# Kernel optimization log

Measured on AMD Instinct MI355X. Metric: run time of the kernel, lower is better.

The kernel has to match this reference:

```python
import jax, jax.numpy as jnp
import numpy as np

N_NODES = 50000
N_EDGES = 200000
N_GRAPHS = 1024
D = 24          # node feature dim (fixed by Set2Set(24))
E_FEAT = 8
E_HID = 128


def setup_inputs() -> dict:
    key = jax.random.key(0)
    ks = jax.random.split(key, 20)
    s = 0.1  # weight scale for numerical sanity
    inp = {
        "x": jax.random.normal(ks[0], (N_NODES, D), jnp.float32),
        "edge_attr": jax.random.normal(ks[1], (N_EDGES, E_FEAT), jnp.float32),
        # edge-network MLP: E_FEAT -> E_HID -> D*D
        "w_e1": jax.random.normal(ks[2], (E_FEAT, E_HID), jnp.float32) * s,
        "b_e1": jnp.zeros((E_HID,), jnp.float32),
        "w_e2": jax.random.normal(ks[3], (E_HID, D * D), jnp.float32) * s,
        "b_e2": jnp.zeros((D * D,), jnp.float32),
        # NNConv root weight + bias
        "root": jax.random.normal(ks[4], (D, D), jnp.float32) * s,
        "bias_conv": jnp.zeros((D,), jnp.float32),
        # Set2Set LSTM (input 2D=48, hidden D=24), torch gate order i,f,g,o
        "w_ih": jax.random.normal(ks[5], (4 * D, 2 * D), jnp.float32) * s,
        "w_hh": jax.random.normal(ks[6], (4 * D, D), jnp.float32) * s,
        "b_ih": jnp.zeros((4 * D,), jnp.float32),
        "b_hh": jnp.zeros((4 * D,), jnp.float32),
        # heads
        "w_fc2": jax.random.normal(ks[7], (2 * D, 8), jnp.float32) * s,
        "b_fc2": jnp.zeros((8,), jnp.float32),
        "w_fc3": jax.random.normal(ks[8], (8, 2), jnp.float32) * s,
        "b_fc3": jnp.zeros((2,), jnp.float32),
        "edge_index": jax.random.randint(ks[9], (2, N_EDGES), 0, N_NODES, jnp.int64),
        "batch": jnp.sort(jax.random.randint(ks[10], (N_NODES,), 0, N_GRAPHS, jnp.int64)),
    }
    return inp


def _nnconv(x, edge_attr, edge_index, w_e1, b_e1, w_e2, b_e2, root, bias_conv):
    src, dst = edge_index[0], edge_index[1]
    h = jax.nn.relu(edge_attr @ w_e1 + b_e1)
    w = (h @ w_e2 + b_e2).reshape(-1, D, D)          # [E, D_in, D_out]
    msg = jnp.einsum('ei,eio->eo', x[src], w)         # gather + per-edge matvec
    s = jax.ops.segment_sum(msg, dst, num_segments=N_NODES)
    cnt = jax.ops.segment_sum(jnp.ones((msg.shape[0],), msg.dtype), dst, num_segments=N_NODES)
    agg = s / jnp.maximum(cnt, 1.0)[:, None]          # scatter-mean
    return agg + x @ root + bias_conv


def _set2set(x, batch, w_ih, w_hh, b_ih, b_hh):
    B = N_GRAPHS
    q_star = jnp.zeros((B, 2 * D), x.dtype)
    h = jnp.zeros((B, D), x.dtype)
    c = jnp.zeros((B, D), x.dtype)
    for _ in range(3):  # processing_steps=3 (fixed small loop)
        gates = q_star @ w_ih.T + b_ih + h @ w_hh.T + b_hh
        i, f, g, o = jnp.split(gates, 4, axis=-1)
        c = jax.nn.sigmoid(f) * c + jax.nn.sigmoid(i) * jnp.tanh(g)
        h = jax.nn.sigmoid(o) * jnp.tanh(c)
        q = h                                         # [B, D]
        e = jnp.sum(x * q[batch], axis=-1)            # [N]
        e_max = jax.ops.segment_max(e, batch, num_segments=B)
        e_max = jnp.where(jnp.isfinite(e_max), e_max, 0.0)
        ex = jnp.exp(e - e_max[batch])
        denom = jax.ops.segment_sum(ex, batch, num_segments=B)
        a = ex / jnp.maximum(denom, 1e-16)[batch]     # per-graph softmax
        r = jax.ops.segment_sum(a[:, None] * x, batch, num_segments=B)
        q_star = jnp.concatenate([q, r], axis=-1)
    return q_star


def reference(x, edge_attr, w_e1, b_e1, w_e2, b_e2, root, bias_conv,
              w_ih, w_hh, b_ih, b_hh, w_fc2, b_fc2, w_fc3, b_fc3,
              edge_index, batch):
    x = _nnconv(x, edge_attr, edge_index, w_e1, b_e1, w_e2, b_e2, root, bias_conv)
    x = jax.nn.relu(x)
    x = _nnconv(x, edge_attr, edge_index, w_e1, b_e1, w_e2, b_e2, root, bias_conv)
    q_star = _set2set(x, batch, w_ih, w_hh, b_ih, b_hh)
    out = jax.nn.relu(q_star @ w_fc2 + b_fc2)
    return out @ w_fc3 + b_fc3                        # [B, 2]
```

## Files before the change

### kernel.cpp

```cpp
#include <hip/hip_runtime.h>
#include <math.h>

#define N_NODES 50000
#define N_EDGES 200000
#define N_GRAPHS 1024
#define DIM 24
#define EF 8
#define EH 128
#define DD 576
#define HSTR 136

typedef __attribute__((ext_vector_type(8))) _Float16 f16x8;
typedef __attribute__((ext_vector_type(4))) _Float16 f16x4;
typedef __attribute__((ext_vector_type(2))) _Float16 f16x2;
typedef __attribute__((ext_vector_type(4))) float float4e;
typedef _Float16 f16;

static __device__ __forceinline__ float sigm(float x) { return 1.0f / (1.0f + expf(-x)); }

__global__ void deg_kernel(const int* __restrict__ dst, int* __restrict__ deg) {
    int i = blockIdx.x * blockDim.x + threadIdx.x;
    if (i < N_EDGES) atomicAdd(&deg[dst[i]], 1);
}

__global__ __launch_bounds__(256) void bz_kernel(const float* __restrict__ w2,
                                                 const float* __restrict__ b2,
                                                 f16* __restrict__ Bz) {
    int idx = blockIdx.x * 256 + threadIdx.x;
    if (idx >= 97 * 2 * 64 * 8) return;
    int kk = idx & 7, lane = (idx >> 3) & 63, nt = (idx >> 9) & 1, p = idx >> 10;
    int q = lane >> 4, l16 = lane & 15, n = nt * 16 + l16;
    float v = 0.0f;
    if (p < 96) {
        int si = p / 24, i = p % 24;
        int k = si * 32 + q * 8 + kk;
        if (n < 24) v = w2[(size_t)k * DD + i * 24 + n];
    } else {
        int i2 = q * 8 + kk;
        if (i2 < 24 && n < 24) v = b2[i2 * 24 + n];
    }
    Bz[idx] = (f16)v;
}

__global__ __launch_bounds__(256, 4) void conv_kernel(
    const float* __restrict__ x, const float* __restrict__ ea,
    const float* __restrict__ w1, const float* __restrict__ b1,
    const f16* __restrict__ Bz,
    const int* __restrict__ src, const int* __restrict__ dst,
    float* __restrict__ agg)
{
    __shared__ f16 hs[128 * HSTR];

    const int t  = threadIdx.x;
    const int e0 = blockIdx.x * 128;

    const int lane = t & 63;
    const int wave = t >> 6;
    const int l16  = lane & 15;
    const int quad = lane >> 4;
    const int ebase = e0 + wave * 32;

    f16x2 xa[12], xb[12];
    {
        int ega = ebase + l16;      if (ega >= N_EDGES) ega = N_EDGES - 1;
        int egb = ebase + 16 + l16; if (egb >= N_EDGES) egb = N_EDGES - 1;
        const float* xra = x + (size_t)src[ega] * DIM;
        const float* xrb = x + (size_t)src[egb] * DIM;
        #pragma unroll
        for (int j4 = 0; j4 < 6; ++j4) {
            float4 va = *(const float4*)(xra + j4 * 4);
            float4 vb = *(const float4*)(xrb + j4 * 4);
            xa[j4 * 2]     = (f16x2){(f16)va.x, (f16)va.y};
            xa[j4 * 2 + 1] = (f16x2){(f16)va.z, (f16)va.w};
            xb[j4 * 2]     = (f16x2){(f16)vb.x, (f16)vb.y};
            xb[j4 * 2 + 1] = (f16x2){(f16)vb.z, (f16)vb.w};
        }
    }

    {
        const int s5 = t & 31;
        const int eb = (t >> 5) * 16;
        float wv[EF][4];
        #pragma unroll
        for (int j = 0; j < EF; ++j) {
            float4 v = *(const float4*)(w1 + j * EH + s5 * 4);
            wv[j][0] = v.x; wv[j][1] = v.y; wv[j][2] = v.z; wv[j][3] = v.w;
        }
        float4 bv = *(const float4*)(b1 + s5 * 4);
        const float bvv[4] = {bv.x, bv.y, bv.z, bv.w};
        #pragma unroll
        for (int e = 0; e < 16; ++e) {
            int eg = e0 + eb + e; if (eg >= N_EDGES) eg = N_EDGES - 1;
            const float* ear = ea + (size_t)eg * EF;
            float4 a0 = *(const float4*)ear;
            float4 a1 = *(const float4*)(ear + 4);
            const float av[EF] = {a0.x, a0.y, a0.z, a0.w, a1.x, a1.y, a1.z, a1.w};
            float r[4] = {bvv[0], bvv[1], bvv[2], bvv[3]};
            #pragma unroll
            for (int j = 0; j < EF; ++j)
                #pragma unroll
                for (int c = 0; c < 4; ++c)
                    r[c] = fmaf(av[j], wv[j][c], r[c]);
            f16x4 hq = { (f16)fmaxf(r[0], 0.0f), (f16)fmaxf(r[1], 0.0f),
                         (f16)fmaxf(r[2], 0.0f), (f16)fmaxf(r[3], 0.0f) };
            *(f16x4*)&hs[(eb + e) * HSTR + s5 * 4] = hq;
        }
    }

    const f16x8* bz = (const f16x8*)Bz + lane;
    f16x8 pb0[2], pb1[2];
    pb0[0] = bz[0];   pb1[0] = bz[64];
    pb0[1] = bz[128]; pb1[1] = bz[192];

    __syncthreads();

    float4e a00 = {0.f,0.f,0.f,0.f}, a01 = {0.f,0.f,0.f,0.f};
    float4e a10 = {0.f,0.f,0.f,0.f}, a11 = {0.f,0.f,0.f,0.f};

    #pragma unroll
    for (int si = 0; si < 4; ++si) {
        union { f16x8 v; f16x2 p[4]; } h0u, h1u;
        h0u.v = *(const f16x8*)&hs[(wave * 32 + l16) * HSTR + si * 32 + quad * 8];
        h1u.v = *(const f16x8*)&hs[(wave * 32 + 16 + l16) * HSTR + si * 32 + quad * 8];
        #pragma unroll
        for (int i = 0; i < 24; ++i) {
            const int p = si * 24 + i;
            f16x8 b0 = pb0[p & 1], b1v = pb1[p & 1];
            if (p + 2 <= 96) {
                pb0[p & 1] = bz[(p + 2) * 128];
                pb1[p & 1] = bz[(p + 2) * 128 + 64];
            }
            f16 xea = (i & 1) ? xa[i >> 1][1] : xa[i >> 1][0];
            f16 xeb = (i & 1) ? xb[i >> 1][1] : xb[i >> 1][0];
            f16x2 xa2 = {xea, xea}, xb2 = {xeb, xeb};
            union { f16x8 v; f16x2 p[4]; } a0u, a1u;
            #pragma unroll
            for (int j = 0; j < 4; ++j) {
                a0u.p[j] = h0u.p[j] * xa2;
                a1u.p[j] = h1u.p[j] * xb2;
            }
            a00 = __builtin_amdgcn_mfma_f32_16x16x32_f16(a0u.v, b0,  a00, 0, 0, 0);
            a10 = __builtin_amdgcn_mfma_f32_16x16x32_f16(a1u.v, b0,  a10, 0, 0, 0);
            a01 = __builtin_amdgcn_mfma_f32_16x16x32_f16(a0u.v, b1v, a01, 0, 0, 0);
            a11 = __builtin_amdgcn_mfma_f32_16x16x32_f16(a1u.v, b1v, a11, 0, 0, 0);
            if ((p % 12) == 11) __syncthreads();
        }
    }

    {
        union { f16x8 v; f16x2 p[4]; } a0u, a1u;
        f16x2 z2 = {(f16)0.f, (f16)0.f};
        if (quad == 0)      { a0u.p[0]=xa[0]; a0u.p[1]=xa[1]; a0u.p[2]=xa[2];  a0u.p[3]=xa[3];
                              a1u.p[0]=xb[0]; a1u.p[1]=xb[1]; a1u.p[2]=xb[2];  a1u.p[3]=xb[3];  }
        else if (quad == 1) { a0u.p[0]=xa[4]; a0u.p[1]=xa[5]; a0u.p[2]=xa[6];  a0u.p[3]=xa[7];
                              a1u.p[0]=xb[4]; a1u.p[1]=xb[5]; a1u.p[2]=xb[6];  a1u.p[3]=xb[7];  }
        else if (quad == 2) { a0u.p[0]=xa[8]; a0u.p[1]=xa[9]; a0u.p[2]=xa[10]; a0u.p[3]=xa[11];
                              a1u.p[0]=xb[8]; a1u.p[1]=xb[9]; a1u.p[2]=xb[10]; a1u.p[3]=xb[11]; }
        else                { a0u.p[0]=z2; a0u.p[1]=z2; a0u.p[2]=z2; a0u.p[3]=z2;
                              a1u.p[0]=z2; a1u.p[1]=z2; a1u.p[2]=z2; a1u.p[3]=z2; }
        a00 = __builtin_amdgcn_mfma_f32_16x16x32_f16(a0u.v, pb0[0], a00, 0, 0, 0);
        a10 = __builtin_amdgcn_mfma_f32_16x16x32_f16(a1u.v, pb0[0], a10, 0, 0, 0);
        a01 = __builtin_amdgcn_mfma_f32_16x16x32_f16(a0u.v, pb1[0], a01, 0, 0, 0);
        a11 = __builtin_amdgcn_mfma_f32_16x16x32_f16(a1u.v, pb1[0], a11, 0, 0, 0);
    }

    #pragma unroll
    for (int r = 0; r < 4; ++r) {
        int er = ebase + quad * 4 + r;
        if (er < N_EDGES) {
            int d = dst[er];
            atomicAdd(&agg[(size_t)d * DIM + l16], a00[r]);
            if (l16 < 8) atomicAdd(&agg[(size_t)d * DIM + 16 + l16], a01[r]);
        }
        int er2 = ebase + 16 + quad * 4 + r;
        if (er2 < N_EDGES) {
            int d = dst[er2];
            atomicAdd(&agg[(size_t)d * DIM + l16], a10[r]);
            if (l16 < 8) atomicAdd(&agg[(size_t)d * DIM + 16 + l16], a11[r]);
        }
    }
}

__global__ void combine_kernel(
    const float* __restrict__ x_in, const float* __restrict__ agg,
    const int* __restrict__ deg, const float* __restrict__ root,
    const float* __restrict__ bias, float* __restrict__ x_out, int do_relu)
{
    int t = blockIdx.x * blockDim.x + threadIdx.x;
    if (t >= N_NODES * DIM) return;
    int v = t / DIM, o = t % DIM;
    int dg = deg[v];
    float d = dg > 0 ? (float)dg : 1.0f;
    float a = agg[t] / d + bias[o];
    const float* xr = x_in + (size_t)v * DIM;
    #pragma unroll
    for (int i = 0; i < DIM; ++i) a = fmaf(xr[i], root[i * DIM + o], a);
    x_out[t] = do_relu ? fmaxf(a, 0.0f) : a;
}

__global__ __launch_bounds__(64) void s2s_kernel(
    const float* __restrict__ x, const int* __restrict__ batch,
    const float* __restrict__ w_ih, const float* __restrict__ w_hh,
    const float* __restrict__ b_ih, const float* __restrict__ b_hh,
    const float* __restrict__ w_fc2, const float* __restrict__ b_fc2,
    const float* __restrict__ w_fc3, const float* __restrict__ b_fc3,
    float* __restrict__ out)
{
    const int g = blockIdx.x;
    const int t = threadIdx.x;
    __shared__ float qs[48];
    __shared__ float hh[24], cc[24], gates[96], zl[8];
    __shared__ int s_lo, s_hi;

    if (t == 0) {
        int lo = 0, hi = N_NODES;
        while (lo < hi) { int m = (lo + hi) >> 1; if (batch[m] < g) lo = m + 1; else hi = m; }
        s_lo = lo;
        int lo2 = lo; hi = N_NODES;
        while (lo2 < hi) { int m = (lo2 + hi) >> 1; if (batch[m] <= g) lo2 = m + 1; else hi = m; }
        s_hi = lo2;
    }
    if (t < 48) qs[t] = 0.0f;
    if (t < 24) { hh[t] = 0.0f; cc[t] = 0.0f; }
    __syncthreads();
    const int lo = s_lo, hi = s_hi;

    for (int it = 0; it < 3; ++it) {
        for (int rr = t; rr < 96; rr += 64) {
            float a = b_ih[rr] + b_hh[rr];
            const float* wi = w_ih + (size_t)rr * 48;
            const float* wh = w_hh + (size_t)rr * 24;
            #pragma unroll
            for (int j = 0; j < 48; ++j) a = fmaf(qs[j], wi[j], a);
            #pragma unroll
            for (int j = 0; j < 24; ++j) a = fmaf(hh[j], wh[j], a);
            gates[rr] = a;
        }
        __syncthreads();
        if (t < 24) {
            float c = sigm(gates[24 + t]) * cc[t] + sigm(gates[t]) * tanhf(gates[48 + t]);
            cc[t] = c;
            float h = sigm(gates[72 + t]) * tanhf(c);
            hh[t] = h;
            qs[t] = h;
        }
        __syncthreads();

        float m_l = -INFINITY, s_l = 0.0f;
        float r_l[24];
        #pragma unroll
        for (int d = 0; d < 24; ++d) r_l[d] = 0.0f;
        for (int n = lo + t; n < hi; n += 64) {
            float xv[24];
            #pragma unroll
            for (int j = 0; j < 6; ++j)
                *(float4*)&xv[j * 4] = ((const float4*)(x + (size_t)n * DIM))[j];
            float e = 0.0f;
            #pragma unroll
            for (int d = 0; d < 24; ++d) e = fmaf(xv[d], qs[d], e);
            if (e > m_l) {
                float sc = expf(m_l - e);
                #pragma unroll
                for (int d = 0; d < 24; ++d) r_l[d] *= sc;
                s_l *= sc;
                m_l = e;
            }
            float w = expf(e - m_l);
            s_l += w;
            #pragma unroll
            for (int d = 0; d < 24; ++d) r_l[d] = fmaf(w, xv[d], r_l[d]);
        }
        float m = m_l;
        #pragma unroll
        for (int off = 32; off; off >>= 1) m = fmaxf(m, __shfl_xor(m, off));
        float fac = (m_l == -INFINITY) ? 0.0f : expf(m_l - m);
        float s = s_l * fac;
        #pragma unroll
        for (int off = 32; off; off >>= 1) s += __shfl_xor(s, off);
        float denom = fmaxf(s, 1e-16f);
        #pragma unroll
        for (int d = 0; d < 24; ++d) {
            float rv = r_l[d] * fac;
            #pragma unroll
            for (int off = 32; off; off >>= 1) rv += __shfl_xor(rv, off);
            if (t == d) qs[24 + d] = rv / denom;
        }
        __syncthreads();
    }

    if (t < 8) {
        float a = b_fc2[t];
        #pragma unroll
        for (int j = 0; j < 48; ++j) a = fmaf(qs[j], w_fc2[j * 8 + t], a);
        zl[t] = fmaxf(a, 0.0f);
    }
    __syncthreads();
    if (t < 2) {
        float a = b_fc3[t];
        #pragma unroll
        for (int k = 0; k < 8; ++k) a = fmaf(zl[k], w_fc3[k * 2 + t], a);
        out[(size_t)g * 2 + t] = a;
    }
}

extern "C" void kernel_launch(void* const* d_in, const int* in_sizes, int n_in,
                              void* d_out, int out_size, void* d_ws, size_t ws_size,
                              hipStream_t stream) {
    const float* x      = (const float*)d_in[0];
    const float* ea     = (const float*)d_in[1];
    const float* w_e1   = (const float*)d_in[2];
    const float* b_e1   = (const float*)d_in[3];
    const float* w_e2   = (const float*)d_in[4];
    const float* b_e2   = (const float*)d_in[5];
    const float* root   = (const float*)d_in[6];
    const float* bias_c = (const float*)d_in[7];
    const float* w_ih   = (const float*)d_in[8];
    const float* w_hh   = (const float*)d_in[9];
    const float* b_ih   = (const float*)d_in[10];
    const float* b_hh   = (const float*)d_in[11];
    const float* w_fc2  = (const float*)d_in[12];
    const float* b_fc2  = (const float*)d_in[13];
    const float* w_fc3  = (const float*)d_in[14];
    const float* b_fc3  = (const float*)d_in[15];
    const int*   eidx   = (const int*)d_in[16];
    const int*   batch  = (const int*)d_in[17];
    const int* esrc = eidx;
    const int* edst = eidx + N_EDGES;
    float* out = (float*)d_out;

    char* ws = (char*)d_ws;
    float* agg   = (float*)(ws);
    int*   deg   = (int*)  (ws + 4800000);
    float* x1    = (float*)(ws + 5789824);
    float* x2    = (float*)(ws + 10589824);
    f16*   Bz    = (f16*)  (ws + 15389824);

    hipMemsetAsync(ws, 0, 5000000, stream);

    deg_kernel<<<(N_EDGES + 255) / 256, 256, 0, stream>>>(edst, deg);
    bz_kernel<<<(97 * 2 * 64 * 8 + 255) / 256, 256, 0, stream>>>(w_e2, b_e2, Bz);

    conv_kernel<<<(N_EDGES + 127) / 128, 256, 0, stream>>>(x, ea, w_e1, b_e1, Bz, esrc, edst, agg);
    combine_kernel<<<(N_NODES * DIM + 255) / 256, 256, 0, stream>>>(x, agg, deg, root, bias_c, x1, 1);

    hipMemsetAsync(agg, 0, 4800000, stream);
    conv_kernel<<<(N_EDGES + 127) / 128, 256, 0, stream>>>(x1, ea, w_e1, b_e1, Bz, esrc, edst, agg);
    combine_kernel<<<(N_NODES * DIM + 255) / 256, 256, 0, stream>>>(x1, agg, deg, root, bias_c, x2, 0);

    s2s_kernel<<<N_GRAPHS, 64, 0, stream>>>(x2, batch, w_ih, w_hh, b_ih, b_hh,
                                            w_fc2, b_fc2, w_fc3, b_fc3, out);
}
```

Baseline: 301.2 us.

## Compute edge hidden layer in registers, fuse prep kernels and agg zeroing

The conv kernel no longer stages the edge-MLP hidden activations in shared memory. Each lane now recomputes its own 8 hidden values per k-slice directly from edge_attr and w_e1, which removes the LDS buffer and all __syncthreads barriers but adds redundant FMAs. The degree and Bz preparation kernels are merged into one launch, and the memset between convs is folded into combine_kernel zeroing agg as it reads it. The s2s gate matvec now uses float4 weight loads.

```diff
diff --git a/kernel.cpp b/kernel.cpp
--- a/kernel.cpp
+++ b/kernel.cpp
@@ -8,25 +8,26 @@
 #define EF 8
 #define EH 128
 #define DD 576
-#define HSTR 136
 
 typedef __attribute__((ext_vector_type(8))) _Float16 f16x8;
-typedef __attribute__((ext_vector_type(4))) _Float16 f16x4;
 typedef __attribute__((ext_vector_type(2))) _Float16 f16x2;
 typedef __attribute__((ext_vector_type(4))) float float4e;
 typedef _Float16 f16;
 
 static __device__ __forceinline__ float sigm(float x) { return 1.0f / (1.0f + expf(-x)); }
 
-__global__ void deg_kernel(const int* __restrict__ dst, int* __restrict__ deg) {
-    int i = blockIdx.x * blockDim.x + threadIdx.x;
-    if (i < N_EDGES) atomicAdd(&deg[dst[i]], 1);
-}
-
-__global__ __launch_bounds__(256) void bz_kernel(const float* __restrict__ w2,
-                                                 const float* __restrict__ b2,
-                                                 f16* __restrict__ Bz) {
-    int idx = blockIdx.x * 256 + threadIdx.x;
+__global__ __launch_bounds__(256) void prep_kernel(
+    const int* __restrict__ dst, int* __restrict__ deg,
+    const float* __restrict__ w2, const float* __restrict__ b2,
+    f16* __restrict__ Bz)
+{
+    const int b = blockIdx.x, t = threadIdx.x;
+    if (b < 782) {
+        int i = b * 256 + t;
+        if (i < N_EDGES) atomicAdd(&deg[dst[i]], 1);
+        return;
+    }
+    int idx = (b - 782) * 256 + t;
     if (idx >= 97 * 2 * 64 * 8) return;
     int kk = idx & 7, lane = (idx >> 3) & 63, nt = (idx >> 9) & 1, p = idx >> 10;
     int q = lane >> 4, l16 = lane & 15, n = nt * 16 + l16;
@@ -49,8 +50,6 @@
     const int* __restrict__ src, const int* __restrict__ dst,
     float* __restrict__ agg)
 {
-    __shared__ f16 hs[128 * HSTR];
-
     const int t  = threadIdx.x;
     const int e0 = blockIdx.x * 128;
 
@@ -60,10 +59,28 @@
     const int quad = lane >> 4;
     const int ebase = e0 + wave * 32;
 
+    const f16x8* bz = (const f16x8*)Bz + lane;
+    f16x8 pb0[2], pb1[2];
+    pb0[0] = bz[0];   pb1[0] = bz[64];
+    pb0[1] = bz[128]; pb1[1] = bz[192];
+
+    int ega = ebase + l16;      if (ega >= N_EDGES) ega = N_EDGES - 1;
+    int egb = ebase + 16 + l16; if (egb >= N_EDGES) egb = N_EDGES - 1;
+
+    float eaa[EF], eab[EF];
+    {
+        const float* pa = ea + (size_t)ega * EF;
+        const float* pb = ea + (size_t)egb * EF;
+        float4 a0 = *(const float4*)pa, a1 = *(const float4*)(pa + 4);
+        float4 b0 = *(const float4*)pb, b1_ = *(const float4*)(pb + 4);
+        eaa[0]=a0.x; eaa[1]=a0.y; eaa[2]=a0.z; eaa[3]=a0.w;
+        eaa[4]=a1.x; eaa[5]=a1.y; eaa[6]=a1.z; eaa[7]=a1.w;
+        eab[0]=b0.x; eab[1]=b0.y; eab[2]=b0.z; eab[3]=b0.w;
+        eab[4]=b1_.x; eab[5]=b1_.y; eab[6]=b1_.z; eab[7]=b1_.w;
+    }
+
     f16x2 xa[12], xb[12];
     {
-        int ega = ebase + l16;      if (ega >= N_EDGES) ega = N_EDGES - 1;
-        int egb = ebase + 16 + l16; if (egb >= N_EDGES) egb = N_EDGES - 1;
         const float* xra = x + (size_t)src[ega] * DIM;
         const float* xrb = x + (size_t)src[egb] * DIM;
         #pragma unroll
@@ -77,51 +94,39 @@
         }
     }
 
-    {
-        const int s5 = t & 31;
-        const int eb = (t >> 5) * 16;
-        float wv[EF][4];
-        #pragma unroll
-        for (int j = 0; j < EF; ++j) {
-            float4 v = *(const float4*)(w1 + j * EH + s5 * 4);
-            wv[j][0] = v.x; wv[j][1] = v.y; wv[j][2] = v.z; wv[j][3] = v.w;
-        }
-        float4 bv = *(const float4*)(b1 + s5 * 4);
-        const float bvv[4] = {bv.x, bv.y, bv.z, bv.w};
-        #pragma unroll
-        for (int e = 0; e < 16; ++e) {
-            int eg = e0 + eb + e; if (eg >= N_EDGES) eg = N_EDGES - 1;
-            const float* ear = ea + (size_t)eg * EF;
-            float4 a0 = *(const float4*)ear;
-            float4 a1 = *(const float4*)(ear + 4);
-            const float av[EF] = {a0.x, a0.y, a0.z, a0.w, a1.x, a1.y, a1.z, a1.w};
-            float r[4] = {bvv[0], bvv[1], bvv[2], bvv[3]};
-            #pragma unroll
-            for (int j = 0; j < EF; ++j)
-                #pragma unroll
-                for (int c = 0; c < 4; ++c)
-                    r[c] = fmaf(av[j], wv[j][c], r[c]);
-            f16x4 hq = { (f16)fmaxf(r[0], 0.0f), (f16)fmaxf(r[1], 0.0f),
-                         (f16)fmaxf(r[2], 0.0f), (f16)fmaxf(r[3], 0.0f) };
-            *(f16x4*)&hs[(eb + e) * HSTR + s5 * 4] = hq;
-        }
-    }
-
-    const f16x8* bz = (const f16x8*)Bz + lane;
-    f16x8 pb0[2], pb1[2];
-    pb0[0] = bz[0];   pb1[0] = bz[64];
-    pb0[1] = bz[128]; pb1[1] = bz[192];
-
-    __syncthreads();
-
     float4e a00 = {0.f,0.f,0.f,0.f}, a01 = {0.f,0.f,0.f,0.f};
     float4e a10 = {0.f,0.f,0.f,0.f}, a11 = {0.f,0.f,0.f,0.f};
 
     #pragma unroll
     for (int si = 0; si < 4; ++si) {
+        const int k0 = si * 32 + quad * 8;
+        float ha[8], hb[8];
+        {
+            float4 bv0 = *(const float4*)(b1 + k0);
+            float4 bv1 = *(const float4*)(b1 + k0 + 4);
+            ha[0]=bv0.x; ha[1]=bv0.y; ha[2]=bv0.z; ha[3]=bv0.w;
+            ha[4]=bv1.x; ha[5]=bv1.y; ha[6]=bv1.z; ha[7]=bv1.w;
+            #pragma unroll
+            for (int kk = 0; kk < 8; ++kk) hb[kk] = ha[kk];
+            #pragma unroll
+            for (int j = 0; j < EF; ++j) {
+                float4 w0 = *(const float4*)(w1 + j * EH + k0);
+                float4 w4 = *(const float4*)(w1 + j * EH + k0 + 4);
+                const float wj[8] = {w0.x, w0.y, w0.z, w0.w, w4.x, w4.y, w4.z, w4.w};
+                #pragma unroll
+                for (int kk = 0; kk < 8; ++kk) {
+                    ha[kk] = fmaf(eaa[j], wj[kk], ha[kk]);
+                    hb[kk] = fmaf(eab[j], wj[kk], hb[kk]);
+                }
+            }
+        }
         union { f16x8 v; f16x2 p[4]; } h0u, h1u;
-        h0u.v = *(const f16x8*)&hs[(wave * 32 + l16) * HSTR + si * 32 + quad * 8];
-        h1u.v = *(const f16x8*)&hs[(wave * 32 + 16 + l16) * HSTR + si * 32 + quad * 8];
+        #pragma unroll
+        for (int kk = 0; kk < 8; ++kk) {
+            ((f16*)&h0u.v)[kk] = (f16)fmaxf(ha[kk], 0.0f);
+            ((f16*)&h1u.v)[kk] = (f16)fmaxf(hb[kk], 0.0f);
+        }
+
         #pragma unroll
         for (int i = 0; i < 24; ++i) {
             const int p = si * 24 + i;
@@ -143,21 +148,18 @@
             a10 = __builtin_amdgcn_mfma_f32_16x16x32_f16(a1u.v, b0,  a10, 0, 0, 0);
             a01 = __builtin_amdgcn_mfma_f32_16x16x32_f16(a0u.v, b1v, a01, 0, 0, 0);
             a11 = __builtin_amdgcn_mfma_f32_16x16x32_f16(a1u.v, b1v, a11, 0, 0, 0);
-            if ((p % 12) == 11) __syncthreads();
         }
     }
 
     {
         union { f16x8 v; f16x2 p[4]; } a0u, a1u;
         f16x2 z2 = {(f16)0.f, (f16)0.f};
-        if (quad == 0)      { a0u.p[0]=xa[0]; a0u.p[1]=xa[1]; a0u.p[2]=xa[2];  a0u.p[3]=xa[3];
-                              a1u.p[0]=xb[0]; a1u.p[1]=xb[1]; a1u.p[2]=xb[2];  a1u.p[3]=xb[3];  }
-        else if (quad == 1) { a0u.p[0]=xa[4]; a0u.p[1]=xa[5]; a0u.p[2]=xa[6];  a0u.p[3]=xa[7];
-                              a1u.p[0]=xb[4]; a1u.p[1]=xb[5]; a1u.p[2]=xb[6];  a1u.p[3]=xb[7];  }
-        else if (quad == 2) { a0u.p[0]=xa[8]; a0u.p[1]=xa[9]; a0u.p[2]=xa[10]; a0u.p[3]=xa[11];
-                              a1u.p[0]=xb[8]; a1u.p[1]=xb[9]; a1u.p[2]=xb[10]; a1u.p[3]=xb[11]; }
-        else                { a0u.p[0]=z2; a0u.p[1]=z2; a0u.p[2]=z2; a0u.p[3]=z2;
-                              a1u.p[0]=z2; a1u.p[1]=z2; a1u.p[2]=z2; a1u.p[3]=z2; }
+        #pragma unroll
+        for (int j = 0; j < 4; ++j) {
+            int i2 = quad * 4 + j;
+            a0u.p[j] = (i2 < 12) ? xa[i2] : z2;
+            a1u.p[j] = (i2 < 12) ? xb[i2] : z2;
+        }
         a00 = __builtin_amdgcn_mfma_f32_16x16x32_f16(a0u.v, pb0[0], a00, 0, 0, 0);
         a10 = __builtin_amdgcn_mfma_f32_16x16x32_f16(a1u.v, pb0[0], a10, 0, 0, 0);
         a01 = __builtin_amdgcn_mfma_f32_16x16x32_f16(a0u.v, pb1[0], a01, 0, 0, 0);
@@ -182,9 +184,10 @@
 }
 
 __global__ void combine_kernel(
-    const float* __restrict__ x_in, const float* __restrict__ agg,
+    const float* __restrict__ x_in, float* __restrict__ agg,
     const int* __restrict__ deg, const float* __restrict__ root,
-    const float* __restrict__ bias, float* __restrict__ x_out, int do_relu)
+    const float* __restrict__ bias, float* __restrict__ x_out,
+    int do_relu, int zero_agg)
 {
     int t = blockIdx.x * blockDim.x + threadIdx.x;
     if (t >= N_NODES * DIM) return;
@@ -192,6 +195,7 @@
     int dg = deg[v];
     float d = dg > 0 ? (float)dg : 1.0f;
     float a = agg[t] / d + bias[o];
+    if (zero_agg) agg[t] = 0.0f;
     const float* xr = x_in + (size_t)v * DIM;
     #pragma unroll
     for (int i = 0; i < DIM; ++i) a = fmaf(xr[i], root[i * DIM + o], a);
@@ -231,9 +235,17 @@
             const float* wi = w_ih + (size_t)rr * 48;
             const float* wh = w_hh + (size_t)rr * 24;
             #pragma unroll
-            for (int j = 0; j < 48; ++j) a = fmaf(qs[j], wi[j], a);
-            #pragma unroll
-            for (int j = 0; j < 24; ++j) a = fmaf(hh[j], wh[j], a);
+            for (int j4 = 0; j4 < 12; ++j4) {
+                float4 w = *(const float4*)(wi + j4 * 4);
+                a = fmaf(qs[j4*4+0], w.x, a); a = fmaf(qs[j4*4+1], w.y, a);
+                a = fmaf(qs[j4*4+2], w.z, a); a = fmaf(qs[j4*4+3], w.w, a);
+            }
+            #pragma unroll
+            for (int j4 = 0; j4 < 6; ++j4) {
+                float4 w = *(const float4*)(wh + j4 * 4);
+                a = fmaf(hh[j4*4+0], w.x, a); a = fmaf(hh[j4*4+1], w.y, a);
+                a = fmaf(hh[j4*4+2], w.z, a); a = fmaf(hh[j4*4+3], w.w, a);
+            }
             gates[rr] = a;
         }
         __syncthreads();
@@ -337,15 +349,13 @@
 
     hipMemsetAsync(ws, 0, 5000000, stream);
 
-    deg_kernel<<<(N_EDGES + 255) / 256, 256, 0, stream>>>(edst, deg);
-    bz_kernel<<<(97 * 2 * 64 * 8 + 255) / 256, 256, 0, stream>>>(w_e2, b_e2, Bz);
+    prep_kernel<<<782 + 388, 256, 0, stream>>>(edst, deg, w_e2, b_e2, Bz);
 
     conv_kernel<<<(N_EDGES + 127) / 128, 256, 0, stream>>>(x, ea, w_e1, b_e1, Bz, esrc, edst, agg);
-    combine_kernel<<<(N_NODES * DIM + 255) / 256, 256, 0, stream>>>(x, agg, deg, root, bias_c, x1, 1);
-
-    hipMemsetAsync(agg, 0, 4800000, stream);
+    combine_kernel<<<(N_NODES * DIM + 255) / 256, 256, 0, stream>>>(x, agg, deg, root, bias_c, x1, 1, 1);
+
     conv_kernel<<<(N_EDGES + 127) / 128, 256, 0, stream>>>(x1, ea, w_e1, b_e1, Bz, esrc, edst, agg);
-    combine_kernel<<<(N_NODES * DIM + 255) / 256, 256, 0, stream>>>(x1, agg, deg, root, bias_c, x2, 0);
+    combine_kernel<<<(N_NODES * DIM + 255) / 256, 256, 0, stream>>>(x1, agg, deg, root, bias_c, x2, 0, 0);
 
     s2s_kernel<<<N_GRAPHS, 64, 0, stream>>>(x2, batch, w_ih, w_hh, b_ih, b_hh,
                                             w_fc2, b_fc2, w_fc3, b_fc3, out);
```

New measurement: 340.3 us. +13.0%, slower.
